# Optimization experiments

Hardware: AMD Instinct MI355X
Metric: run time of the kernel (lower is better)

The kernel has to match this reference:

```python
import jax, jax.numpy as jnp
import numpy as np

LN_EPS = 1e-5
NEG_INF = -1e30


def setup_inputs() -> dict:
    key = jax.random.key(0)
    k_adj, k_feat, k_mask, k_w = jax.random.split(key, 4)
    B, N, H, R, L = 8, 400, 768, 46, 2
    adj = jax.random.uniform(k_adj, (B, N, N, R), dtype=jnp.float32)
    feature = jax.random.normal(k_feat, (B, N, H), dtype=jnp.float32)
    dmask = (jax.random.uniform(k_mask, (B, 1, N)) > 0.1).astype(jnp.float32)
    # per-layer, per-relation Linear(H, H, bias=False) weights, applied as x @ W
    W = jax.random.normal(k_w, (L, R, H, H), dtype=jnp.float32) / np.sqrt(H)
    return {"adj": adj, "feature": feature, "dmask": dmask, "W": W}


def reference(adj, feature, dmask, W):
    # adj: [B,N,N,R] -> [B,R,N,N]; dmask: [B,1,N] masks key/column axis
    B, N, _, R = adj.shape
    a = jnp.transpose(adj, (0, 3, 1, 2))           # [B,R,N,N]
    m = dmask[:, None, :, :]                        # [B,1,1,N]
    logits = a * m + (1.0 - m) * NEG_INF
    att = jax.nn.softmax(logits, axis=-1)           # [B,R,N,N] (layer-invariant)

    x = feature
    num_layers = W.shape[0]
    for layer in range(num_layers):
        # grouped per-relation linear: h[b,r,n,k] = feature[b,n,h] @ W[layer,r,h,k]
        h = jnp.einsum('bnh,rhk->brnk', x, W[layer])
        h = jax.nn.relu(jnp.einsum('brnm,brmk->brnk', att, h))
        addition = h.sum(axis=1)                    # sum over relations -> [B,N,H]
        z = jax.nn.relu(addition) / R
        # LayerNorm without affine params
        mu = jnp.mean(z, axis=-1, keepdims=True)
        var = jnp.var(z, axis=-1, keepdims=True)
        x = (z - mu) / jnp.sqrt(var + LN_EPS)
        # dropout is identity in eval mode
    return x
```

## Files before the change

### kernel.cpp

```cpp
#include <hip/hip_runtime.h>
#include <stdint.h>

#define BS 8
#define NN 400
#define HH 768
#define RR 46
#define MPAD 416
#define MFLAT2 3328
#define LDW2 3328
#define PADM 402

typedef _Float16 half8 __attribute__((ext_vector_type(8)));
typedef _Float16 half4v __attribute__((ext_vector_type(4)));
typedef float floatx4 __attribute__((ext_vector_type(4)));

__device__ __forceinline__ void async16(const void* g, void* l) {
  __builtin_amdgcn_global_load_lds((const __attribute__((address_space(1))) uint32_t*)g,
                                   (__attribute__((address_space(3))) uint32_t*)l, 16, 0, 0);
}

__device__ __forceinline__ int xcd_work(int flat, int nwg) {
  int q = nwg >> 3, rem = nwg & 7;
  int xcd = flat & 7, slot = flat >> 3;
  return (xcd < rem ? xcd * (q + 1) : rem * (q + 1) + (xcd - rem) * q) + slot;
}

__device__ __forceinline__ void vm_wait(int ahead) {
  if (ahead >= 2) asm volatile("s_waitcnt vmcnt(8)" ::: "memory");
  else if (ahead == 1) asm volatile("s_waitcnt vmcnt(4)" ::: "memory");
  else asm volatile("s_waitcnt vmcnt(0)" ::: "memory");
}
__device__ __forceinline__ void vm_wait2(int ahead) {
  if (ahead >= 2) asm volatile("s_waitcnt vmcnt(4)" ::: "memory");
  else if (ahead == 1) asm volatile("s_waitcnt vmcnt(2)" ::: "memory");
  else asm volatile("s_waitcnt vmcnt(0)" ::: "memory");
}
#define BAR_ONE() { asm volatile("s_barrier" ::: "memory"); __builtin_amdgcn_sched_barrier(0); }


__device__ __forceinline__ void mma32(const _Float16* As, const _Float16* Bs, int lane,
                                      int wr, int wc, floatx4 acc[8][4]) {
  int arow = wr + (lane & 15);
  int brow = wc + (lane & 15);
  int kswz = ((lane >> 4) ^ ((lane >> 1) & 3)) * 8;
  half8 a[8], b[4];
#pragma unroll
  for (int i = 0; i < 8; ++i) a[i] = *(const half8*)&As[(arow + i * 16) * 32 + kswz];
#pragma unroll
  for (int j = 0; j < 4; ++j) b[j] = *(const half8*)&Bs[(brow + j * 16) * 32 + kswz];
#pragma unroll
  for (int i = 0; i < 8; ++i)
#pragma unroll
    for (int j = 0; j < 4; ++j)
      acc[i][j] = __builtin_amdgcn_mfma_f32_16x16x32_f16(a[i], b[j], acc[i][j], 0, 0, 0);
}

__device__ __forceinline__ void mma8(const _Float16* As, const _Float16* Bs, int lane,
                                     int wr, int wc, floatx4 acc[4][2]) {
  int arow = wr + (lane & 15);
  int brow = wc + (lane & 15);
  int kswz = ((lane >> 4) ^ ((lane >> 1) & 3)) * 8;
  half8 a[4], b[2];
#pragma unroll
  for (int i = 0; i < 4; ++i) a[i] = *(const half8*)&As[(arow + i * 16) * 32 + kswz];
#pragma unroll
  for (int j = 0; j < 2; ++j) b[j] = *(const half8*)&Bs[(brow + j * 16) * 32 + kswz];
#pragma unroll
  for (int i = 0; i < 4; ++i)
#pragma unroll
    for (int j = 0; j < 2; ++j)
      acc[i][j] = __builtin_amdgcn_mfma_f32_16x16x32_f16(a[i], b[j], acc[i][j], 0, 0, 0);
}

__global__ __launch_bounds__(256) void conv_w(const float* __restrict__ W, _Float16* __restrict__ Wt) {
  __shared__ float tl[32][33];
  int t = threadIdx.x;
  int lr = blockIdx.y;
  int tr = blockIdx.x / 24, tc = blockIdx.x % 24;
  const float* src = W + (size_t)lr * HH * HH;
  _Float16* dst = Wt + (size_t)lr * HH * HH;
  int rl = t >> 5, cl = t & 31;
#pragma unroll
  for (int j = 0; j < 4; ++j)
    tl[rl + 8 * j][cl] = src[(size_t)(tr * 32 + rl + 8 * j) * HH + tc * 32 + cl];
  __syncthreads();
#pragma unroll
  for (int j = 0; j < 4; ++j)
    dst[(size_t)(tc * 32 + rl + 8 * j) * HH + tr * 32 + cl] = (_Float16)tl[cl][rl + 8 * j];
}

__global__ void conv_x(const float* __restrict__ f, _Float16* __restrict__ x16) {
  int i4 = blockIdx.x * 256 + threadIdx.x;
  int row = i4 / 192;
  int c4 = i4 - row * 192;
  int b = row / 416;
  int m = row - b * 416;
  half4v h = {};
  if (m < NN) {
    float4 v = *(const float4*)(f + ((size_t)(b * NN + m) * HH) + c4 * 4);
    h[0] = (_Float16)v.x; h[1] = (_Float16)v.y; h[2] = (_Float16)v.z; h[3] = (_Float16)v.w;
  }
  *(half4v*)&x16[(size_t)row * HH + c4 * 4] = h;
}

__global__ __launch_bounds__(512) void att_softmax(const float* __restrict__ adj,
                                                   const float* __restrict__ dmask,
                                                   _Float16* __restrict__ att) {
  __shared__ _Float16 sE[RR * PADM];
  __shared__ float sM[NN];
  int t = threadIdx.x;
  int n = blockIdx.x, b = blockIdx.y;
  const float4* src = (const float4*)(adj + ((size_t)b * NN + n) * NN * RR);
  for (int i = t; i < NN; i += 512) sM[i] = dmask[b * NN + i];
  float4 v[9];
#pragma unroll
  for (int k = 0; k < 9; ++k) {
    int idx = t + k * 512;
    if (idx < NN * RR / 4) v[k] = src[idx];
  }
  __syncthreads();
#pragma unroll
  for (int k = 0; k < 9; ++k) {
    int idx = t + k * 512;
    if (idx < NN * RR / 4) {
      int e0 = idx * 4;
      float vv[4] = {v[k].x, v[k].y, v[k].z, v[k].w};
#pragma unroll
      for (int j = 0; j < 4; ++j) {
        int e = e0 + j;
        int m = e / RR;
        int r = e - m * RR;
        float val = sM[m] > 0.5f ? __expf(vv[j]) : 0.0f;
        sE[r * PADM + m] = (_Float16)val;
      }
    }
  }
  __syncthreads();
  int lane = t & 63, wid = t >> 6;
  for (int r = wid; r < RR; r += 8) {
    const _Float16* row = &sE[r * PADM];
    float s = 0.f;
    for (int m = lane; m < NN; m += 64) s += (float)row[m];
#pragma unroll
    for (int o = 32; o; o >>= 1) s += __shfl_xor(s, o);
    float inv = 1.0f / s;
    _Float16* orow = att + (((size_t)b * RR + r) * NN + n) * MPAD;
    for (int m2 = lane * 2; m2 < MPAD; m2 += 128) {
      _Float16 lo = (_Float16)0.f, hi = (_Float16)0.f;
      if (m2 < NN) lo = (_Float16)((float)row[m2] * inv);
      if (m2 + 1 < NN) hi = (_Float16)((float)row[m2 + 1] * inv);
      union { _Float16 h[2]; uint32_t u; } pk;
      pk.h[0] = lo; pk.h[1] = hi;
      *(uint32_t*)&orow[m2] = pk.u;
    }
  }
}

__global__ __launch_bounds__(512, 2) void gemm_xw(const _Float16* __restrict__ x16,
                                                  const _Float16* __restrict__ Wt,
                                                  _Float16* __restrict__ h1T, int layer, int r0, int rbase) {
  extern __shared__ __align__(16) char smraw[];
  int t = threadIdx.x;
  int work = xcd_work(blockIdx.x, gridDim.x);
  int r_i = work / 39;
  int rem = work - r_i * 39;
  int r = r0 + r_i;
  int mtile = rem / 3, ntile = rem % 3;
  const _Float16* Bp = Wt + ((size_t)layer * RR + r) * HH * HH;
  int lane = t & 63, w = t >> 6;
  int wr = (w >> 2) * 128, wc = (w & 3) * 64;
  floatx4 acc[8][4] = {};

  int c0 = w * 2;
  int swz = ((lane & 3) ^ ((lane >> 3) & 3)) * 8;
  int ra0 = mtile * 256 + c0 * 16 + (lane >> 2);
  int ra1 = ra0 + 16;
  int rb0 = ntile * 256 + c0 * 16 + (lane >> 2);
  int rb1 = rb0 + 16;
  const _Float16* pa0 = x16 + (size_t)ra0 * HH + swz;
  const _Float16* pa1 = x16 + (size_t)ra1 * HH + swz;
  const _Float16* pb0 = Bp + (size_t)rb0 * HH + swz;
  const _Float16* pb1 = Bp + (size_t)rb1 * HH + swz;
  auto issue = [&](int buf) {
    _Float16* lA = (_Float16*)(smraw + (buf << 15)) + c0 * 512;
    _Float16* lB = (_Float16*)(smraw + (buf << 15) + 16384) + c0 * 512;
    async16(pa0, lA); async16(pa1, lA + 512);
    async16(pb0, lB); async16(pb1, lB + 512);
    pa0 += 32; pa1 += 32; pb0 += 32; pb1 += 32;
  };

  issue(0); issue(1); issue(2);
  vm_wait(2);
  BAR_ONE();
  for (int s = 0; s < 24; ++s) {
    if (s + 3 < 24) issue((s + 3) & 3);
    char* cb = smraw + ((s & 3) << 15);
    __builtin_amdgcn_s_setprio(1);
    mma32((const _Float16*)cb, (const _Float16*)(cb + 16384), lane, wr, wc, acc);
    __builtin_amdgcn_s_setprio(0);
    if (s + 1 < 24) {
      int ahead = 24 - s - 2;
      vm_wait(ahead > 2 ? 2 : ahead);
      BAR_ONE();
    }
  }
  __syncthreads();

  _Float16* outl = (_Float16*)smraw + (size_t)w * 8192;
#pragma unroll
  for (int i = 0; i < 8; ++i) {
#pragma unroll
    for (int j = 0; j < 4; ++j) {
      int rl = i * 16 + (lane >> 4) * 4;
      int cl = j * 16 + (lane & 15);
      int pos = rl ^ ((cl & 7) << 3);
      half4v v = {(_Float16)acc[i][j][0], (_Float16)acc[i][j][1],
                  (_Float16)acc[i][j][2], (_Float16)acc[i][j][3]};
      *(half4v*)&outl[cl * 128 + pos] = v;
    }
  }
  _Float16* outp = h1T + (size_t)(r - rbase) * HH * LDW2;
  int gmb = mtile * 256 + wr;
  int gnb = ntile * 256 + wc;
#pragma unroll
  for (int p = 0; p < 16; ++p) {
    int c = p * 4 + (lane >> 4);
    int mq = (lane & 15) * 8;
    int mpos = mq ^ ((c & 7) << 3);
    half8 v = *(const half8*)&outl[c * 128 + mpos];
    *(half8*)&outp[(size_t)(gnb + c) * LDW2 + gmb + mq] = v;
  }
}

__global__ __launch_bounds__(512, 4) void gemm_att(const _Float16* __restrict__ att,
                                                   const _Float16* __restrict__ h1T,
                                                   float* __restrict__ partials, size_t psz,
                                                   int rs, int rcount, int rbase, int accflag,
                                                   int ngroups) {
  __shared__ __align__(16) char smraw[65536];
  int t = threadIdx.x;
  int work = xcd_work(blockIdx.x, gridDim.x);
  int ntile = work % 6;
  int tmp = work / 6;
  int mtile = tmp & 3; tmp >>= 2;
  int g = tmp % ngroups;
  int b = tmp / ngroups;
  int rbeg = rs + (g * rcount) / ngroups;
  int rend = rs + ((g + 1) * rcount) / ngroups;
  int nr = rend - rbeg;
  int total = nr * 13;
  float* part = partials + (size_t)g * psz;
  int lane = t & 63, w = t >> 6;
  int wr = (w >> 2) * 64, wc = (w & 3) * 32;
  floatx4 acc[4][2] = {}, sum[4][2] = {};

  int srow = w * 16 + (lane >> 2);
  int scol = ((lane & 3) ^ ((lane >> 3) & 3)) * 8;
  int ga = mtile * 128 + srow; ga = ga > NN - 1 ? NN - 1 : ga;
  int gb = ntile * 128 + srow;
  const _Float16* pa = att + ((size_t)b * RR + rbeg) * NN * MPAD + (size_t)ga * MPAD + scol;
  const _Float16* pb = h1T + (size_t)(rbeg - rbase) * HH * LDW2 + (size_t)gb * LDW2 + b * MPAD + scol;
  int nsk = 0;
  auto issue = [&](int buf) {
    char* lb = smraw + (buf << 14) + w * 1024;
    async16(pa, lb);
    async16(pb, lb + 8192);
    if (++nsk == 13) { nsk = 0; pa += (size_t)NN * MPAD - 384; pb += (size_t)HH * LDW2 - 384; }
    else { pa += 32; pb += 32; }
  };

  issue(0); issue(1); issue(2);
  vm_wait2(2);
  BAR_ONE();
  int cks = 0;
  for (int s = 0; s < total; ++s) {
    if (s + 3 < total) issue((s + 3) & 3);
    char* cb = smraw + ((s & 3) << 14);
    __builtin_amdgcn_s_setprio(1);
    mma8((const _Float16*)cb, (const _Float16*)(cb + 8192), lane, wr, wc, acc);
    __builtin_amdgcn_s_setprio(0);
    if (cks == 12) {
#pragma unroll
      for (int i = 0; i < 4; ++i)
#pragma unroll
        for (int j = 0; j < 2; ++j) {
#pragma unroll
          for (int q2 = 0; q2 < 4; ++q2) sum[i][j][q2] += fmaxf(acc[i][j][q2], 0.0f);
          acc[i][j] = (floatx4){0.f, 0.f, 0.f, 0.f};
        }
      cks = 0;
    } else ++cks;
    if (s + 1 < total) {
      int ahead = total - s - 2;
      vm_wait2(ahead > 2 ? 2 : ahead);
      BAR_ONE();
    }
  }
#pragma unroll
  for (int i = 0; i < 4; ++i) {
    int rl = wr + i * 16 + (lane >> 4) * 4;
    int grow = mtile * 128 + rl;
#pragma unroll
    for (int j = 0; j < 2; ++j) {
      int gcol = ntile * 128 + wc + j * 16 + (lane & 15);
#pragma unroll
      for (int q2 = 0; q2 < 4; ++q2) {
        if (grow + q2 < NN) {
          size_t idx = ((size_t)b * NN + grow + q2) * HH + gcol;
          float v = sum[i][j][q2];
          if (accflag) v += part[idx];
          part[idx] = v;
        }
      }
    }
  }
}

__global__ __launch_bounds__(256) void lnorm(const float* __restrict__ partials, size_t psz, int np,
                                             _Float16* __restrict__ x16, float* __restrict__ out) {
  int row = blockIdx.x;
  int t = threadIdx.x;
  int b = row / NN;
  int xrow = row + b * 16;
  float v[3];
  float s = 0.f, s2 = 0.f;
#pragma unroll
  for (int j = 0; j < 3; ++j) {
    float a = 0.f;
    for (int gidx = 0; gidx < np; ++gidx) a += partials[(size_t)gidx * psz + (size_t)row * HH + t + j * 256];
    v[j] = fmaxf(a, 0.f) * (1.0f / RR);
    s += v[j];
    s2 += v[j] * v[j];
  }
#pragma unroll
  for (int o = 32; o; o >>= 1) {
    s += __shfl_xor(s, o);
    s2 += __shfl_xor(s2, o);
  }
  __shared__ float rs_[4], rs2_[4];
  int lane = t & 63, wid = t >> 6;
  if (!lane) { rs_[wid] = s; rs2_[wid] = s2; }
  __syncthreads();
  s = rs_[0] + rs_[1] + rs_[2] + rs_[3];
  s2 = rs2_[0] + rs2_[1] + rs2_[2] + rs2_[3];
  float mu = s * (1.0f / HH);
  float var = s2 * (1.0f / HH) - mu * mu;
  float rstd = rsqrtf(var + 1e-5f);
#pragma unroll
  for (int j = 0; j < 3; ++j) {
    float o = (v[j] - mu) * rstd;
    out[(size_t)row * HH + t + j * 256] = o;
    x16[(size_t)xrow * HH + t + j * 256] = (_Float16)o;
  }
}

extern "C" void kernel_launch(void* const* d_in, const int* in_sizes, int n_in,
                              void* d_out, int out_size, void* d_ws, size_t ws_size,
                              hipStream_t stream) {
  const float* adj = (const float*)d_in[0];
  const float* feature = (const float*)d_in[1];
  const float* dmask = (const float*)d_in[2];
  const float* W = (const float*)d_in[3];
  float* out = (float*)d_out;

  (void)hipFuncSetAttribute((const void*)gemm_xw,
                            hipFuncAttributeMaxDynamicSharedMemorySize, 131072);

  uintptr_t base = (uintptr_t)d_ws;
  uintptr_t p = base;
  auto alloc = [&](size_t bytes) -> void* {
    uintptr_t q = (p + 255) & ~(uintptr_t)255;
    p = q + bytes;
    return (void*)q;
  };
  _Float16* att = (_Float16*)alloc((size_t)BS * RR * NN * MPAD * 2);
  _Float16* Wt = (_Float16*)alloc((size_t)2 * RR * HH * HH * 2);
  _Float16* x16 = (_Float16*)alloc((size_t)MFLAT2 * HH * 2);
  size_t psz = (size_t)(BS * NN) * HH;
  size_t pszB = psz * 4;
  size_t used = p - base;
  size_t rem = ws_size > used ? ws_size - used : 0;
  size_t perR = (size_t)HH * LDW2 * 2;
  size_t h1full = (size_t)RR * perR;

  conv_w<<<dim3(576, 2 * RR), 256, 0, stream>>>(W, Wt);
  conv_x<<<MFLAT2 * HH / 4 / 256, 256, 0, stream>>>(feature, x16);
  att_softmax<<<dim3(NN, BS), 512, 0, stream>>>(adj, dmask, att);

  if (rem >= h1full + 4 * pszB + 512) {
    _Float16* h1T = (_Float16*)alloc(h1full);
    int ngroups = (int)(((ws_size - (p - base)) - 256) / pszB);
    if (ngroups > 8) ngroups = 8;
    float* partials = (float*)alloc((size_t)ngroups * pszB);
    for (int layer = 0; layer < 2; ++layer) {
      gemm_xw<<<39 * RR, 512, 131072, stream>>>(x16, Wt, h1T, layer, 0, 0);
      gemm_att<<<6 * 4 * ngroups * BS, 512, 0, stream>>>(att, h1T, partials, psz, 0, RR, 0, 0, ngroups);
      lnorm<<<BS * NN, 256, 0, stream>>>(partials, psz, ngroups, x16, out);
    }
  } else {
    float* partials = (float*)alloc(pszB);
    size_t rem2 = ws_size > (p - base) ? ws_size - (p - base) : 0;
    int RCmax = (int)(rem2 / perR);
    if (RCmax > RR) RCmax = RR;
    if (RCmax < 1) RCmax = 1;
    _Float16* h1T = (_Float16*)alloc((size_t)RCmax * perR);
    for (int layer = 0; layer < 2; ++layer) {
      for (int r0 = 0; r0 < RR; r0 += RCmax) {
        int rc = RR - r0 < RCmax ? RR - r0 : RCmax;
        gemm_xw<<<39 * rc, 512, 131072, stream>>>(x16, Wt, h1T, layer, r0, r0);
        gemm_att<<<6 * 4 * 1 * BS, 512, 0, stream>>>(att, h1T, partials, psz, r0, rc, r0, r0 > 0, 1);
      }
      lnorm<<<BS * NN, 256, 0, stream>>>(partials, psz, 1, x16, out);
    }
  }
}
```

Measured before the change: 1.008 ms.

## Enlarge gemm_att output tile to 256x128 with per-wave 64x64 subtiles

The attention GEMM's M tile grows from 128 to 256 rows, so the four M tiles with padding waste become two, and each wave now computes a 64x64 block (4x4 MFMAs) instead of 64x32. This improves operand reuse per LDS load and halves the number of workgroups that reload the same h1T B tiles. In exchange it uses 96KB of dynamic LDS for the 4-stage buffers, launch bounds drop to 2 blocks per CU, accumulator registers double, and the grid halves, which can lower occupancy and parallelism.

```diff
diff --git a/kernel.cpp b/kernel.cpp
--- a/kernel.cpp
+++ b/kernel.cpp
@@ -30,13 +30,30 @@
   else if (ahead == 1) asm volatile("s_waitcnt vmcnt(4)" ::: "memory");
   else asm volatile("s_waitcnt vmcnt(0)" ::: "memory");
 }
-__device__ __forceinline__ void vm_wait2(int ahead) {
-  if (ahead >= 2) asm volatile("s_waitcnt vmcnt(4)" ::: "memory");
-  else if (ahead == 1) asm volatile("s_waitcnt vmcnt(2)" ::: "memory");
+__device__ __forceinline__ void vm_wait3(int ahead) {
+  if (ahead >= 2) asm volatile("s_waitcnt vmcnt(6)" ::: "memory");
+  else if (ahead == 1) asm volatile("s_waitcnt vmcnt(3)" ::: "memory");
   else asm volatile("s_waitcnt vmcnt(0)" ::: "memory");
 }
 #define BAR_ONE() { asm volatile("s_barrier" ::: "memory"); __builtin_amdgcn_sched_barrier(0); }
 
+
+__device__ __forceinline__ void mma_tiles(const _Float16* As, const _Float16* Bs, int lane,
+                                          int wr, int wc, floatx4 acc[4][4]) {
+  int arow = wr + (lane & 15);
+  int brow = wc + (lane & 15);
+  int kswz = ((lane >> 4) ^ ((lane >> 1) & 3)) * 8;
+  half8 a[4], b[4];
+#pragma unroll
+  for (int i = 0; i < 4; ++i) a[i] = *(const half8*)&As[(arow + i * 16) * 32 + kswz];
+#pragma unroll
+  for (int i = 0; i < 4; ++i) b[i] = *(const half8*)&Bs[(brow + i * 16) * 32 + kswz];
+#pragma unroll
+  for (int i = 0; i < 4; ++i)
+#pragma unroll
+    for (int j = 0; j < 4; ++j)
+      acc[i][j] = __builtin_amdgcn_mfma_f32_16x16x32_f16(a[i], b[j], acc[i][j], 0, 0, 0);
+}
 
 __device__ __forceinline__ void mma32(const _Float16* As, const _Float16* Bs, int lane,
                                       int wr, int wc, floatx4 acc[8][4]) {
@@ -52,23 +69,6 @@
   for (int i = 0; i < 8; ++i)
 #pragma unroll
     for (int j = 0; j < 4; ++j)
-      acc[i][j] = __builtin_amdgcn_mfma_f32_16x16x32_f16(a[i], b[j], acc[i][j], 0, 0, 0);
-}
-
-__device__ __forceinline__ void mma8(const _Float16* As, const _Float16* Bs, int lane,
-                                     int wr, int wc, floatx4 acc[4][2]) {
-  int arow = wr + (lane & 15);
-  int brow = wc + (lane & 15);
-  int kswz = ((lane >> 4) ^ ((lane >> 1) & 3)) * 8;
-  half8 a[4], b[2];
-#pragma unroll
-  for (int i = 0; i < 4; ++i) a[i] = *(const half8*)&As[(arow + i * 16) * 32 + kswz];
-#pragma unroll
-  for (int j = 0; j < 2; ++j) b[j] = *(const half8*)&Bs[(brow + j * 16) * 32 + kswz];
-#pragma unroll
-  for (int i = 0; i < 4; ++i)
-#pragma unroll
-    for (int j = 0; j < 2; ++j)
       acc[i][j] = __builtin_amdgcn_mfma_f32_16x16x32_f16(a[i], b[j], acc[i][j], 0, 0, 0);
 }
 
@@ -232,17 +232,17 @@
   }
 }
 
-__global__ __launch_bounds__(512, 4) void gemm_att(const _Float16* __restrict__ att,
+__global__ __launch_bounds__(512, 2) void gemm_att(const _Float16* __restrict__ att,
                                                    const _Float16* __restrict__ h1T,
                                                    float* __restrict__ partials, size_t psz,
                                                    int rs, int rcount, int rbase, int accflag,
                                                    int ngroups) {
-  __shared__ __align__(16) char smraw[65536];
+  extern __shared__ __align__(16) char smraw[];
   int t = threadIdx.x;
   int work = xcd_work(blockIdx.x, gridDim.x);
   int ntile = work % 6;
   int tmp = work / 6;
-  int mtile = tmp & 3; tmp >>= 2;
+  int mtile = tmp & 1; tmp >>= 1;
   int g = tmp % ngroups;
   int b = tmp / ngroups;
   int rbeg = rs + (g * rcount) / ngroups;
@@ -251,39 +251,46 @@
   int total = nr * 13;
   float* part = partials + (size_t)g * psz;
   int lane = t & 63, w = t >> 6;
-  int wr = (w >> 2) * 64, wc = (w & 3) * 32;
-  floatx4 acc[4][2] = {}, sum[4][2] = {};
-
-  int srow = w * 16 + (lane >> 2);
-  int scol = ((lane & 3) ^ ((lane >> 3) & 3)) * 8;
-  int ga = mtile * 128 + srow; ga = ga > NN - 1 ? NN - 1 : ga;
-  int gb = ntile * 128 + srow;
-  const _Float16* pa = att + ((size_t)b * RR + rbeg) * NN * MPAD + (size_t)ga * MPAD + scol;
-  const _Float16* pb = h1T + (size_t)(rbeg - rbase) * HH * LDW2 + (size_t)gb * LDW2 + b * MPAD + scol;
+  int wr = (w >> 1) * 64, wc = (w & 1) * 64;
+  floatx4 acc[4][4] = {}, sum[4][4] = {};
+
+  int swz = ((lane & 3) ^ ((lane >> 3) & 3)) * 8;
+  int ga0 = mtile * 256 + w * 32 + (lane >> 2);
+  int ga1 = ga0 + 16;
+  ga0 = ga0 > NN - 1 ? NN - 1 : ga0;
+  ga1 = ga1 > NN - 1 ? NN - 1 : ga1;
+  int gb = ntile * 128 + w * 16 + (lane >> 2);
+  const _Float16* pa0 = att + ((size_t)b * RR + rbeg) * NN * MPAD + (size_t)ga0 * MPAD + swz;
+  const _Float16* pa1 = att + ((size_t)b * RR + rbeg) * NN * MPAD + (size_t)ga1 * MPAD + swz;
+  const _Float16* pb = h1T + (size_t)(rbeg - rbase) * HH * LDW2 + (size_t)gb * LDW2 + b * MPAD + swz;
   int nsk = 0;
   auto issue = [&](int buf) {
-    char* lb = smraw + (buf << 14) + w * 1024;
-    async16(pa, lb);
-    async16(pb, lb + 8192);
-    if (++nsk == 13) { nsk = 0; pa += (size_t)NN * MPAD - 384; pb += (size_t)HH * LDW2 - 384; }
-    else { pa += 32; pb += 32; }
+    _Float16* lA = (_Float16*)(smraw + buf * 24576) + (w * 2) * 512;
+    _Float16* lB = (_Float16*)(smraw + buf * 24576 + 16384) + w * 512;
+    async16(pa0, lA); async16(pa1, lA + 512);
+    async16(pb, lB);
+    if (++nsk == 13) {
+      nsk = 0;
+      pa0 += (size_t)NN * MPAD - 384; pa1 += (size_t)NN * MPAD - 384;
+      pb += (size_t)HH * LDW2 - 384;
+    } else { pa0 += 32; pa1 += 32; pb += 32; }
   };
 
   issue(0); issue(1); issue(2);
-  vm_wait2(2);
+  vm_wait3(2);
   BAR_ONE();
   int cks = 0;
   for (int s = 0; s < total; ++s) {
     if (s + 3 < total) issue((s + 3) & 3);
-    char* cb = smraw + ((s & 3) << 14);
+    char* cb = smraw + (s & 3) * 24576;
     __builtin_amdgcn_s_setprio(1);
-    mma8((const _Float16*)cb, (const _Float16*)(cb + 8192), lane, wr, wc, acc);
+    mma_tiles((const _Float16*)cb, (const _Float16*)(cb + 16384), lane, wr, wc, acc);
     __builtin_amdgcn_s_setprio(0);
     if (cks == 12) {
 #pragma unroll
       for (int i = 0; i < 4; ++i)
 #pragma unroll
-        for (int j = 0; j < 2; ++j) {
+        for (int j = 0; j < 4; ++j) {
 #pragma unroll
           for (int q2 = 0; q2 < 4; ++q2) sum[i][j][q2] += fmaxf(acc[i][j][q2], 0.0f);
           acc[i][j] = (floatx4){0.f, 0.f, 0.f, 0.f};
@@ -292,16 +299,16 @@
     } else ++cks;
     if (s + 1 < total) {
       int ahead = total - s - 2;
-      vm_wait2(ahead > 2 ? 2 : ahead);
+      vm_wait3(ahead > 2 ? 2 : ahead);
       BAR_ONE();
     }
   }
 #pragma unroll
   for (int i = 0; i < 4; ++i) {
     int rl = wr + i * 16 + (lane >> 4) * 4;
-    int grow = mtile * 128 + rl;
-#pragma unroll
-    for (int j = 0; j < 2; ++j) {
+    int grow = mtile * 256 + rl;
+#pragma unroll
+    for (int j = 0; j < 4; ++j) {
       int gcol = ntile * 128 + wc + j * 16 + (lane & 15);
 #pragma unroll
       for (int q2 = 0; q2 < 4; ++q2) {
@@ -365,6 +372,8 @@
 
   (void)hipFuncSetAttribute((const void*)gemm_xw,
                             hipFuncAttributeMaxDynamicSharedMemorySize, 131072);
+  (void)hipFuncSetAttribute((const void*)gemm_att,
+                            hipFuncAttributeMaxDynamicSharedMemorySize, 98304);
 
   uintptr_t base = (uintptr_t)d_ws;
   uintptr_t p = base;
@@ -394,7 +403,7 @@
     float* partials = (float*)alloc((size_t)ngroups * pszB);
     for (int layer = 0; layer < 2; ++layer) {
       gemm_xw<<<39 * RR, 512, 131072, stream>>>(x16, Wt, h1T, layer, 0, 0);
-      gemm_att<<<6 * 4 * ngroups * BS, 512, 0, stream>>>(att, h1T, partials, psz, 0, RR, 0, 0, ngroups);
+      gemm_att<<<96 * ngroups, 512, 98304, stream>>>(att, h1T, partials, psz, 0, RR, 0, 0, ngroups);
       lnorm<<<BS * NN, 256, 0, stream>>>(partials, psz, ngroups, x16, out);
     }
   } else {
@@ -408,7 +417,7 @@
       for (int r0 = 0; r0 < RR; r0 += RCmax) {
         int rc = RR - r0 < RCmax ? RR - r0 : RCmax;
         gemm_xw<<<39 * rc, 512, 131072, stream>>>(x16, Wt, h1T, layer, r0, r0);
-        gemm_att<<<6 * 4 * 1 * BS, 512, 0, stream>>>(att, h1T, partials, psz, r0, rc, r0, r0 > 0, 1);
+        gemm_att<<<96 * 1, 512, 98304, stream>>>(att, h1T, partials, psz, r0, rc, r0, r0 > 0, 1);
       }
       lnorm<<<BS * NN, 256, 0, stream>>>(partials, psz, 1, x16, out);
     }
```

After: 987.3 us. 1.02x faster.
